# Optimization experiments

Hardware: AMD Instinct MI355X
Metric: run time of the kernel (lower is better)

## Reference

```python
import jax, jax.numpy as jnp
import numpy as np

N = 1048576
D = 128
NUM_GRAPHS = 4096

def setup_inputs() -> dict:
    key = jax.random.key(0)
    k1, k2 = jax.random.split(key)
    x = jax.random.normal(k1, (N, D), dtype=jnp.float32)
    batch = jnp.sort(jax.random.randint(k2, (N,), 0, NUM_GRAPHS, dtype=jnp.int64))
    return {"x": x, "batch": batch, "num_graphs": NUM_GRAPHS}

def reference(x, batch, num_graphs):
    # Single-pass scatter-mean: segment_sum of features and of counts.
    seg_sum = jax.ops.segment_sum(x, batch, num_segments=num_graphs)          # (B, D)
    counts = jax.ops.segment_sum(jnp.ones((x.shape[0],), x.dtype), batch,
                                 num_segments=num_graphs)                      # (B,)
    # Avoid div-by-zero for (rare) empty segments; torch would yield NaN there.
    safe = jnp.maximum(counts, 1.0)
    return seg_sum / safe[:, None]
```

## Files before the change

### kernel.cpp

```cpp
#include <hip/hip_runtime.h>
#include <hip/hip_bf16.h>


#define D       128
#define D4      32
#define THREADS 256
#define RIF     8
#define UNROLL  4

typedef float v4f __attribute__((ext_vector_type(4)));

__device__ __forceinline__ int lower_bound_dev(const int* __restrict__ a,
                                               int lo, int hi, int v) {
    while (lo < hi) {
        int mid = (lo + hi) >> 1;
        if (a[mid] < v) lo = mid + 1; else hi = mid;
    }
    return lo;
}

__global__ __launch_bounds__(THREADS)
void pool_mean_kernel(const v4f* __restrict__ x,
                      const int* __restrict__ batch,
                      float* __restrict__ out,
                      int n_rows) {
    const int s = blockIdx.x;

    const int lo = lower_bound_dev(batch, 0, n_rows, s);
    const int hi = lower_bound_dev(batch, lo, n_rows, s + 1);
    const int cnt = hi - lo;
    const float inv = 1.0f / (float)(cnt > 1 ? cnt : 1);

    const int col = threadIdx.x & (D4 - 1);
    const int rl  = threadIdx.x >> 5;

    v4f acc = (v4f){0.f, 0.f, 0.f, 0.f};

    int i = lo + rl;
    const v4f* p = x + (size_t)i * D4 + col;
    for (; i + (UNROLL - 1) * RIF < hi; i += UNROLL * RIF) {
        v4f v0 = __builtin_nontemporal_load(p + 0 * RIF * D4);
        v4f v1 = __builtin_nontemporal_load(p + 1 * RIF * D4);
        v4f v2 = __builtin_nontemporal_load(p + 2 * RIF * D4);
        v4f v3 = __builtin_nontemporal_load(p + 3 * RIF * D4);
        acc += v0; acc += v1; acc += v2; acc += v3;
        p += UNROLL * RIF * D4;
    }
    for (; i < hi; i += RIF) {
        acc += __builtin_nontemporal_load(p);
        p += RIF * D4;
    }

    __shared__ v4f partials[RIF][D4];
    partials[rl][col] = acc;
    __syncthreads();

    if (threadIdx.x < D4) {
        v4f t = partials[0][col];
        #pragma unroll
        for (int r = 1; r < RIF; ++r) t += partials[r][col];
        t *= inv;
        v4f* o = (v4f*)out + (size_t)s * D4 + col;
        __builtin_nontemporal_store(t, o);
    }
}

extern "C" void kernel_launch(void* const* d_in, const int* in_sizes, int n_in,
                              void* d_out, int out_size, void* d_ws, size_t ws_size,
                              hipStream_t stream) {
    const v4f* x      = (const v4f*)d_in[0];
    const int* batch  = (const int*)d_in[1];
    float* out        = (float*)d_out;

    const int n_rows     = in_sizes[0] / D;
    const int num_graphs = out_size / D;

    pool_mean_kernel<<<num_graphs, THREADS, 0, stream>>>(x, batch, out, n_rows);
}
```

Baseline: 656.5 us.

## Precompute segment starts in a separate kernel and unroll the row loop deeper

Each block no longer runs two binary searches over the sorted batch array. A small pre-kernel now writes segment start offsets into workspace by detecting boundaries between adjacent batch entries, and the reduction kernel reads lo and hi directly. The main loop unroll also goes from 4 to 8, putting more loads in flight per thread. The cost is an extra kernel launch and a pass over the 4 MB batch array, plus higher register pressure from the deeper unroll.

```diff
diff --git a/kernel.cpp b/kernel.cpp
--- a/kernel.cpp
+++ b/kernel.cpp
@@ -6,28 +6,32 @@
 #define D4      32
 #define THREADS 256
 #define RIF     8
-#define UNROLL  4
+#define UNROLL  8
 
 typedef float v4f __attribute__((ext_vector_type(4)));
 
-__device__ __forceinline__ int lower_bound_dev(const int* __restrict__ a,
-                                               int lo, int hi, int v) {
-    while (lo < hi) {
-        int mid = (lo + hi) >> 1;
-        if (a[mid] < v) lo = mid + 1; else hi = mid;
+__global__ __launch_bounds__(256)
+void find_starts_kernel(const int* __restrict__ batch,
+                        int* __restrict__ starts,
+                        int n_rows, int num_graphs) {
+    int i = blockIdx.x * blockDim.x + threadIdx.x;
+    if (i >= n_rows) return;
+    int b    = batch[i];
+    int prev = (i == 0) ? -1 : batch[i - 1];
+    for (int s = prev + 1; s <= b; ++s) starts[s] = i;
+    if (i == n_rows - 1) {
+        for (int s = b + 1; s <= num_graphs; ++s) starts[s] = n_rows;
     }
-    return lo;
 }
 
 __global__ __launch_bounds__(THREADS)
 void pool_mean_kernel(const v4f* __restrict__ x,
-                      const int* __restrict__ batch,
-                      float* __restrict__ out,
-                      int n_rows) {
+                      const int* __restrict__ starts,
+                      float* __restrict__ out) {
     const int s = blockIdx.x;
 
-    const int lo = lower_bound_dev(batch, 0, n_rows, s);
-    const int hi = lower_bound_dev(batch, lo, n_rows, s + 1);
+    const int lo  = starts[s];
+    const int hi  = starts[s + 1];
     const int cnt = hi - lo;
     const float inv = 1.0f / (float)(cnt > 1 ? cnt : 1);
 
@@ -43,7 +47,12 @@
         v4f v1 = __builtin_nontemporal_load(p + 1 * RIF * D4);
         v4f v2 = __builtin_nontemporal_load(p + 2 * RIF * D4);
         v4f v3 = __builtin_nontemporal_load(p + 3 * RIF * D4);
+        v4f v4 = __builtin_nontemporal_load(p + 4 * RIF * D4);
+        v4f v5 = __builtin_nontemporal_load(p + 5 * RIF * D4);
+        v4f v6 = __builtin_nontemporal_load(p + 6 * RIF * D4);
+        v4f v7 = __builtin_nontemporal_load(p + 7 * RIF * D4);
         acc += v0; acc += v1; acc += v2; acc += v3;
+        acc += v4; acc += v5; acc += v6; acc += v7;
         p += UNROLL * RIF * D4;
     }
     for (; i < hi; i += RIF) {
@@ -71,9 +80,12 @@
     const v4f* x      = (const v4f*)d_in[0];
     const int* batch  = (const int*)d_in[1];
     float* out        = (float*)d_out;
+    int* starts       = (int*)d_ws;
 
     const int n_rows     = in_sizes[0] / D;
     const int num_graphs = out_size / D;
 
-    pool_mean_kernel<<<num_graphs, THREADS, 0, stream>>>(x, batch, out, n_rows);
+    find_starts_kernel<<<(n_rows + 255) / 256, 256, 0, stream>>>(
+        batch, starts, n_rows, num_graphs);
+    pool_mean_kernel<<<num_graphs, THREADS, 0, stream>>>(x, starts, out);
 }
```

After: 648.5 us. About the same (-1.2%).
